# Kernel tuning notes

Hardware: AMD Instinct MI355X
Metric: run time of the kernel (lower is better)

## Reference

```python
import jax, jax.numpy as jnp
import numpy as np

N = 100000      # num_nodes
FEAT = 256      # num_features
H = 128         # hidden
C = 40          # num_classes
K = 4           # hops
RWS = 10        # random-walk samples per node
NL = 2          # nlayer
ALPHA = 0.1


def setup_inputs() -> dict:
    key = jax.random.key(0)
    ks = jax.random.split(key, 10)
    x = jax.random.normal(ks[0], (N, FEAT), dtype=jnp.float32)
    degree = jax.random.uniform(ks[1], (N,), minval=1.0, maxval=64.0, dtype=jnp.float32)
    # precomputed random-walk endpoints per layer per hop: [NL, K, N*RWS]
    ends = jax.random.randint(ks[2], (NL, K, N * RWS), 0, N, dtype=jnp.int32)
    # att init: alpha*(1-alpha)^k, last entry (1-alpha)^K, tiled per layer
    a = ALPHA * (1.0 - ALPHA) ** jnp.arange(K + 1, dtype=jnp.float32)
    a = a.at[-1].set((1.0 - ALPHA) ** K)
    att = jnp.tile(a[None, :], (NL, 1))
    def lin(k, fan_in, fan_out):
        s = 1.0 / np.sqrt(fan_in)
        return jax.random.uniform(k, (fan_in, fan_out), minval=-s, maxval=s, dtype=jnp.float32)
    W0 = lin(ks[3], FEAT, H)
    b0 = jnp.zeros((H,), dtype=jnp.float32)
    W1 = lin(ks[4], H, H)
    b1 = jnp.zeros((H,), dtype=jnp.float32)
    W2 = lin(ks[5], H, C)
    b2 = jnp.zeros((C,), dtype=jnp.float32)
    return {"x": x, "degree": degree, "ends": ends, "att": att,
            "W0": W0, "b0": b0, "W1": W1, "b1": b1, "W2": W2, "b2": b2}


def reference(x, degree, ends, att, W0, b0, W1, b1, W2, b2):
    Ws = [(W0, b0), (W1, b1)]
    starts = jnp.repeat(jnp.arange(N), RWS)          # [N*RWS] walk start node ids
    d_sqrt = jnp.sqrt(degree)                        # degree^0.5
    d_isqrt = jax.lax.rsqrt(degree)                  # degree^-0.5
    h = x
    for i in range(NL):
        W, b = Ws[i]
        h = h @ W + b                                # Linear (dropout p=0)
        mask = att[i]                                # [K+1]
        agg = h * mask[0]
        for k in range(1, K + 1):
            e = ends[i, k - 1]                       # [N*RWS] hop-k endpoints
            w = d_sqrt[starts] * d_isqrt[e]          # degree reweighting
            samp = (w[:, None] * h[e]).reshape(N, RWS, h.shape[1]).mean(axis=1)
            agg = agg + samp * mask[k]
        h = jax.nn.relu(agg)
    logits = h @ W2 + b2
    return jax.nn.log_softmax(logits, axis=1)
```

## Files before the change

kernel.cpp:

```cpp
#include <hip/hip_runtime.h>
#include <math.h>

#define NNODES 100000
#define NFEAT  256
#define HID    128
#define NCLS   40
#define KHOP   4
#define RWSAMP 10
#define KP1    5

typedef __bf16 bf16;
typedef __attribute__((ext_vector_type(8)))  __bf16 bf16x8;
typedef __attribute__((ext_vector_type(2)))  float  f32x2;
typedef __attribute__((ext_vector_type(16))) float  f32x16;

__global__ __launch_bounds__(256) void prep_w(
    const float* __restrict__ W0, const float* __restrict__ W1,
    const float* __restrict__ W2,
    bf16* __restrict__ Wt0, bf16* __restrict__ Wt1, bf16* __restrict__ Wt2)
{
    int tid = blockIdx.x * 256 + threadIdx.x;
    if (tid < 128 * 256) {
        int n = tid >> 8, k = tid & 255;
        Wt0[tid] = (bf16)W0[k * 128 + n];
    } else if (tid < 128 * 256 + 128 * 128) {
        int i = tid - 128 * 256;
        int n = i >> 7, k = i & 127;
        Wt1[i] = (bf16)W1[k * 128 + n];
    } else if (tid < 128 * 256 + 128 * 128 + 64 * 128) {
        int i = tid - (128 * 256 + 128 * 128);
        int n = i >> 7, k = i & 127;
        Wt2[i] = (n < NCLS) ? (bf16)W2[k * NCLS + n] : (bf16)0.0f;
    }
}

template<int K, bool A_BF16>
__global__ __launch_bounds__(256) void gemm_nodes(
    const void* __restrict__ Av, const bf16* __restrict__ Wt,
    const float* __restrict__ bias, unsigned char* __restrict__ F8, int M)
{
    constexpr int BK  = 128;
    constexpr int LDB = BK + 4;
    __shared__ bf16 Bs[128 * LDB];
    __shared__ bf16 As[4][32 * LDB];

    const int tid  = threadIdx.x;
    const int wv   = tid >> 6;
    const int lane = tid & 63;
    const int l31  = lane & 31;
    const int lhi  = lane >> 5;
    const int blockRow = blockIdx.x * 128;
    const int rowBase  = blockRow + wv * 32;

    const bf16*  Ab = (const bf16*)Av;
    const float* Af = (const float*)Av;

    f32x16 acc[4];
#pragma unroll
    for (int t = 0; t < 4; ++t)
#pragma unroll
        for (int r = 0; r < 16; ++r) acc[t][r] = 0.0f;

    for (int k0 = 0; k0 < K; k0 += BK) {
        if (k0) __syncthreads();
#pragma unroll 4
        for (int l = 0; l < 8; ++l) {
            int c   = tid + l * 256;
            int row = c >> 4;
            int kc  = (c & 15) * 8;
            uint4 v = *(const uint4*)(Wt + (size_t)row * K + k0 + kc);
            *(uint2*)&Bs[row * LDB + kc]     = make_uint2(v.x, v.y);
            *(uint2*)&Bs[row * LDB + kc + 4] = make_uint2(v.z, v.w);
        }
        __syncthreads();

        if (A_BF16) {
#pragma unroll 4
            for (int l = 0; l < 8; ++l) {
                int c  = lane + l * 64;
                int r  = c >> 4;
                int kc = (c & 15) * 8;
                int gr = min(rowBase + r, M - 1);
                uint4 v = *(const uint4*)(Ab + (size_t)gr * K + k0 + kc);
                *(uint2*)&As[wv][r * LDB + kc]     = make_uint2(v.x, v.y);
                *(uint2*)&As[wv][r * LDB + kc + 4] = make_uint2(v.z, v.w);
            }
        } else {
#pragma unroll 4
            for (int l = 0; l < 16; ++l) {
                int c  = lane + l * 64;
                int r  = c >> 5;
                int kc = (c & 31) * 4;
                int gr = min(rowBase + r, M - 1);
                float4 v = *(const float4*)(Af + (size_t)gr * K + k0 + kc);
                union { bf16 h[4]; uint2 u; } t4;
                t4.h[0] = (bf16)v.x; t4.h[1] = (bf16)v.y;
                t4.h[2] = (bf16)v.z; t4.h[3] = (bf16)v.w;
                *(uint2*)&As[wv][r * LDB + kc] = t4.u;
            }
        }

#pragma unroll
        for (int ks = 0; ks < BK / 16; ++ks) {
            const int ko = ks * 16 + lhi * 8;
            union { uint2 u2[2]; bf16x8 v; } ua, ub;
            ua.u2[0] = *(const uint2*)&As[wv][l31 * LDB + ko];
            ua.u2[1] = *(const uint2*)&As[wv][l31 * LDB + ko + 4];
            bf16x8 a = ua.v;
#pragma unroll
            for (int t = 0; t < 4; ++t) {
                ub.u2[0] = *(const uint2*)&Bs[(t * 32 + l31) * LDB + ko];
                ub.u2[1] = *(const uint2*)&Bs[(t * 32 + l31) * LDB + ko + 4];
                acc[t] = __builtin_amdgcn_mfma_f32_32x32x16_bf16(a, ub.v, acc[t], 0, 0, 0);
            }
        }
    }

    __syncthreads();
    unsigned* ldsq = (unsigned*)Bs;

#pragma unroll
    for (int t = 0; t < 4; ++t) {
        int col = t * 32 + l31;
        float bc = bias[col];
#pragma unroll
        for (int G = 0; G < 4; ++G) {
            float v0 = acc[t][4 * G + 0] + bc;
            float v1 = acc[t][4 * G + 1] + bc;
            float v2 = acc[t][4 * G + 2] + bc;
            float v3 = acc[t][4 * G + 3] + bc;
            int p = __builtin_amdgcn_cvt_pk_fp8_f32(v0, v1, 0, false);
            p = __builtin_amdgcn_cvt_pk_fp8_f32(v2, v3, p, true);
            ldsq[(wv * 8 + 2 * G + lhi) * 128 + col] = (unsigned)p;
        }
    }
    __syncthreads();

    {
        const int j  = tid & 31;
        const int Q0 = (tid >> 5) * 4;
#pragma unroll
        for (int qq = 0; qq < 4; ++qq) {
            int Q = Q0 + qq;
            uint4 d = *(const uint4*)&ldsq[Q * 128 + 4 * j];
            int growb = blockRow + 4 * Q;
#pragma unroll
            for (int i = 0; i < 4; ++i) {
                unsigned sel = ((unsigned)(4 + i) << 8) | (unsigned)i;
                unsigned lo = __builtin_amdgcn_perm(d.y, d.x, sel);
                unsigned hi = __builtin_amdgcn_perm(d.w, d.z, sel);
                unsigned o  = __builtin_amdgcn_perm(hi, lo, 0x05040100u);
                if (growb + i < M)
                    *(unsigned*)(F8 + (size_t)(growb + i) * 128 + 4 * j) = o;
            }
        }
    }
}

__global__ __launch_bounds__(256) void agg_relu_fp8(
    const unsigned char* __restrict__ hf8, bf16* __restrict__ hout,
    const int* __restrict__ ends, const float* __restrict__ degree,
    const float* __restrict__ att)
{
    __shared__ int2 sew[4][40];

    const int wv   = threadIdx.x >> 6;
    const int lane = threadIdx.x & 63;
    const int n    = blockIdx.x * 4 + wv;

    if (lane < KHOP * RWSAMP) {
        int k = lane / RWSAMP, s = lane - k * RWSAMP;
        int e = ends[(size_t)k * (NNODES * RWSAMP) + (size_t)n * RWSAMP + s];
        float w = att[k + 1] * (1.0f / RWSAMP) * sqrtf(degree[n]) * rsqrtf(degree[e]);
        sew[wv][lane] = make_int2(e << 7, __float_as_int(w));
    }

    const int q  = lane >> 4;
    const int c8 = (lane & 15) * 8;

    f32x2 a0 = {0.f, 0.f}, a1 = {0.f, 0.f}, a2 = {0.f, 0.f}, a3 = {0.f, 0.f};

#pragma unroll
    for (int t = 0; t < 10; ++t) {
        int2  ew   = sew[wv][4 * t + q];
        unsigned v = (unsigned)ew.x + (unsigned)c8;
        float wj   = __int_as_float(ew.y);
        f32x2 w2   = {wj, wj};
        uint2 g = *(const uint2*)(hf8 + v);
        a0 = __builtin_elementwise_fma(w2, __builtin_amdgcn_cvt_pk_f32_fp8((int)g.x, false), a0);
        a1 = __builtin_elementwise_fma(w2, __builtin_amdgcn_cvt_pk_f32_fp8((int)g.x, true),  a1);
        a2 = __builtin_elementwise_fma(w2, __builtin_amdgcn_cvt_pk_f32_fp8((int)g.y, false), a2);
        a3 = __builtin_elementwise_fma(w2, __builtin_amdgcn_cvt_pk_f32_fp8((int)g.y, true),  a3);
    }

    a0.x += __shfl_xor(a0.x, 16, 64); a0.y += __shfl_xor(a0.y, 16, 64);
    a1.x += __shfl_xor(a1.x, 16, 64); a1.y += __shfl_xor(a1.y, 16, 64);
    a2.x += __shfl_xor(a2.x, 16, 64); a2.y += __shfl_xor(a2.y, 16, 64);
    a3.x += __shfl_xor(a3.x, 16, 64); a3.y += __shfl_xor(a3.y, 16, 64);
    a0.x += __shfl_xor(a0.x, 32, 64); a0.y += __shfl_xor(a0.y, 32, 64);
    a1.x += __shfl_xor(a1.x, 32, 64); a1.y += __shfl_xor(a1.y, 32, 64);
    a2.x += __shfl_xor(a2.x, 32, 64); a2.y += __shfl_xor(a2.y, 32, 64);
    a3.x += __shfl_xor(a3.x, 32, 64); a3.y += __shfl_xor(a3.y, 32, 64);

    if (q == 0) {
        float att0 = att[0];
        f32x2 av = {att0, att0};
        unsigned vs = ((unsigned)n << 7) + (unsigned)c8;
        uint2 sv = *(const uint2*)(hf8 + vs);
        a0 = __builtin_elementwise_fma(av, __builtin_amdgcn_cvt_pk_f32_fp8((int)sv.x, false), a0);
        a1 = __builtin_elementwise_fma(av, __builtin_amdgcn_cvt_pk_f32_fp8((int)sv.x, true),  a1);
        a2 = __builtin_elementwise_fma(av, __builtin_amdgcn_cvt_pk_f32_fp8((int)sv.y, false), a2);
        a3 = __builtin_elementwise_fma(av, __builtin_amdgcn_cvt_pk_f32_fp8((int)sv.y, true),  a3);

        f32x2 z = {0.f, 0.f};
        a0 = __builtin_elementwise_max(a0, z);
        a1 = __builtin_elementwise_max(a1, z);
        a2 = __builtin_elementwise_max(a2, z);
        a3 = __builtin_elementwise_max(a3, z);

        union { bf16 h[8]; uint4 u; } st;
        st.h[0] = (bf16)a0.x; st.h[1] = (bf16)a0.y;
        st.h[2] = (bf16)a1.x; st.h[3] = (bf16)a1.y;
        st.h[4] = (bf16)a2.x; st.h[5] = (bf16)a2.y;
        st.h[6] = (bf16)a3.x; st.h[7] = (bf16)a3.y;
        *(uint4*)(hout + (size_t)n * HID + c8) = st.u;
    }
}

__global__ __launch_bounds__(256) void head_mfma(
    const bf16* __restrict__ h, const bf16* __restrict__ Wt2,
    const float* __restrict__ b2, float* __restrict__ out, int M)
{
    constexpr int K = HID, LDB = K + 8;
    __shared__ bf16 Bs[64 * LDB];

    const int tid = threadIdx.x;
    constexpr int CPR = K / 8;
    for (int f = tid; f < 64 * CPR; f += 256) {
        int row = f / CPR;
        int kc  = (f % CPR) * 8;
        *(uint4*)&Bs[row * LDB + kc] = *(const uint4*)(Wt2 + (size_t)row * K + kc);
    }
    __syncthreads();

    const int wv   = tid >> 6;
    const int lane = tid & 63;
    const int l31  = lane & 31;
    const int lhi  = lane >> 5;
    const int blockRow = blockIdx.x * 128;
    const int arow = min(blockRow + wv * 32 + l31, M - 1);

    f32x16 acc[2];
#pragma unroll
    for (int t = 0; t < 2; ++t)
#pragma unroll
        for (int r = 0; r < 16; ++r) acc[t][r] = 0.0f;

#pragma unroll
    for (int ks = 0; ks < K / 16; ++ks) {
        bf16x8 a = *(const bf16x8*)(h + (size_t)arow * K + ks * 16 + lhi * 8);
#pragma unroll
        for (int t = 0; t < 2; ++t) {
            bf16x8 b = *(const bf16x8*)&Bs[(t * 32 + l31) * LDB + ks * 16 + lhi * 8];
            acc[t] = __builtin_amdgcn_mfma_f32_32x32x16_bf16(a, b, acc[t], 0, 0, 0);
        }
    }

    const float bc0 = b2[l31];
    const float bc1 = (l31 < 8) ? b2[32 + l31] : 0.0f;

#pragma unroll
    for (int r = 0; r < 16; ++r) {
        float v0 = acc[0][r] + bc0;
        float v1 = (l31 < 8) ? (acc[1][r] + bc1) : -INFINITY;

        float m = fmaxf(v0, v1);
#pragma unroll
        for (int off = 16; off > 0; off >>= 1)
            m = fmaxf(m, __shfl_xor(m, off, 64));

        float s = __expf(v0 - m) + ((l31 < 8) ? __expf(v1 - m) : 0.0f);
#pragma unroll
        for (int off = 16; off > 0; off >>= 1)
            s += __shfl_xor(s, off, 64);

        float ls = __logf(s);
        int grow = blockRow + wv * 32 + (r & 3) + 8 * (r >> 2) + 4 * lhi;
        if (grow < M) {
            out[(size_t)grow * NCLS + l31] = v0 - m - ls;
            if (l31 < 8)
                out[(size_t)grow * NCLS + 32 + l31] = v1 - m - ls;
        }
    }
}

extern "C" void kernel_launch(void* const* d_in, const int* in_sizes, int n_in,
                              void* d_out, int out_size, void* d_ws, size_t ws_size,
                              hipStream_t stream)
{
    const float* x      = (const float*)d_in[0];
    const float* degree = (const float*)d_in[1];
    const int*   ends   = (const int*)  d_in[2];
    const float* att    = (const float*)d_in[3];
    const float* W0     = (const float*)d_in[4];
    const float* b0     = (const float*)d_in[5];
    const float* W1     = (const float*)d_in[6];
    const float* b1     = (const float*)d_in[7];
    const float* W2     = (const float*)d_in[8];
    const float* b2     = (const float*)d_in[9];
    float* out = (float*)d_out;

    bf16* hb0 = (bf16*)d_ws;
    bf16* hb1 = hb0 + (size_t)NNODES * HID;
    unsigned char* hf8 = (unsigned char*)(hb1 + (size_t)NNODES * HID);
    bf16* Wt0 = (bf16*)(hf8 + (size_t)NNODES * HID);
    bf16* Wt1 = Wt0 + 128 * 256;
    bf16* Wt2 = Wt1 + 128 * 128;

    const int prepN = 128 * 256 + 128 * 128 + 64 * 128;
    prep_w<<<(prepN + 255) / 256, 256, 0, stream>>>(W0, W1, W2, Wt0, Wt1, Wt2);

    const int gGemm = (NNODES + 127) / 128;

    gemm_nodes<NFEAT, false><<<gGemm, 256, 0, stream>>>(x, Wt0, b0, hf8, NNODES);
    agg_relu_fp8<<<NNODES / 4, 256, 0, stream>>>(hf8, hb1, ends, degree, att);
    gemm_nodes<HID, true><<<gGemm, 256, 0, stream>>>(hb1, Wt1, b1, hf8, NNODES);
    agg_relu_fp8<<<NNODES / 4, 256, 0, stream>>>(
        hf8, hb0, ends + (size_t)KHOP * NNODES * RWSAMP, degree, att + KP1);
    head_mfma<<<gGemm, 256, 0, stream>>>(hb0, Wt2, b2, out, NNODES);
}
```

Baseline: 351.3 us.

## Fuse random-walk aggregation into following GEMM and head kernels via LDS

Aggregation+ReLU is merged into the layer-1 GEMM kernel and into the classifier head kernel. Aggregated rows for a 64-node tile are staged as bf16 in shared memory instead of written to a global bf16 buffer and read back. This removes two launches and the global round trip of the intermediate activations. In exchange each wave handles 16 nodes serially in the gather phase, B operands are read straight from global memory, and half the waves idle in the head GEMM.

```diff
diff --git a/kernel.cpp b/kernel.cpp
--- a/kernel.cpp
+++ b/kernel.cpp
@@ -13,6 +13,8 @@
 typedef __attribute__((ext_vector_type(8)))  __bf16 bf16x8;
 typedef __attribute__((ext_vector_type(2)))  float  f32x2;
 typedef __attribute__((ext_vector_type(16))) float  f32x16;
+
+#define LDA 132
 
 __global__ __launch_bounds__(256) void prep_w(
     const float* __restrict__ W0, const float* __restrict__ W1,
@@ -34,13 +36,11 @@
     }
 }
 
-template<int K, bool A_BF16>
-__global__ __launch_bounds__(256) void gemm_nodes(
-    const void* __restrict__ Av, const bf16* __restrict__ Wt,
+__global__ __launch_bounds__(256) void gemm0(
+    const float* __restrict__ Af, const bf16* __restrict__ Wt,
     const float* __restrict__ bias, unsigned char* __restrict__ F8, int M)
 {
-    constexpr int BK  = 128;
-    constexpr int LDB = BK + 4;
+    constexpr int K = NFEAT, BK = 128, LDB = BK + 4;
     __shared__ bf16 Bs[128 * LDB];
     __shared__ bf16 As[4][32 * LDB];
 
@@ -51,9 +51,6 @@
     const int lhi  = lane >> 5;
     const int blockRow = blockIdx.x * 128;
     const int rowBase  = blockRow + wv * 32;
-
-    const bf16*  Ab = (const bf16*)Av;
-    const float* Af = (const float*)Av;
 
     f32x16 acc[4];
 #pragma unroll
@@ -74,30 +71,17 @@
         }
         __syncthreads();
 
-        if (A_BF16) {
 #pragma unroll 4
-            for (int l = 0; l < 8; ++l) {
-                int c  = lane + l * 64;
-                int r  = c >> 4;
-                int kc = (c & 15) * 8;
-                int gr = min(rowBase + r, M - 1);
-                uint4 v = *(const uint4*)(Ab + (size_t)gr * K + k0 + kc);
-                *(uint2*)&As[wv][r * LDB + kc]     = make_uint2(v.x, v.y);
-                *(uint2*)&As[wv][r * LDB + kc + 4] = make_uint2(v.z, v.w);
-            }
-        } else {
-#pragma unroll 4
-            for (int l = 0; l < 16; ++l) {
-                int c  = lane + l * 64;
-                int r  = c >> 5;
-                int kc = (c & 31) * 4;
-                int gr = min(rowBase + r, M - 1);
-                float4 v = *(const float4*)(Af + (size_t)gr * K + k0 + kc);
-                union { bf16 h[4]; uint2 u; } t4;
-                t4.h[0] = (bf16)v.x; t4.h[1] = (bf16)v.y;
-                t4.h[2] = (bf16)v.z; t4.h[3] = (bf16)v.w;
-                *(uint2*)&As[wv][r * LDB + kc] = t4.u;
-            }
+        for (int l = 0; l < 16; ++l) {
+            int c  = lane + l * 64;
+            int r  = c >> 5;
+            int kc = (c & 31) * 4;
+            int gr = min(rowBase + r, M - 1);
+            float4 v = *(const float4*)(Af + (size_t)gr * K + k0 + kc);
+            union { bf16 h[4]; uint2 u; } t4;
+            t4.h[0] = (bf16)v.x; t4.h[1] = (bf16)v.y;
+            t4.h[2] = (bf16)v.z; t4.h[3] = (bf16)v.w;
+            *(uint2*)&As[wv][r * LDB + kc] = t4.u;
         }
 
 #pragma unroll
@@ -157,98 +141,102 @@
     }
 }
 
-__global__ __launch_bounds__(256) void agg_relu_fp8(
-    const unsigned char* __restrict__ hf8, bf16* __restrict__ hout,
+__device__ __forceinline__ void agg_phase(
+    bf16* As, int2 (*sew)[40],
+    const unsigned char* __restrict__ f8in,
+    const int* __restrict__ ends, const float* __restrict__ degree,
+    const float* __restrict__ att, int blockRow, int wv, int lane)
+{
+    int hopoff = 0; float aw = 0.0f;
+    if (lane < KHOP * RWSAMP) {
+        int k = lane / RWSAMP, s = lane - k * RWSAMP;
+        hopoff = k * (NNODES * RWSAMP) + s;
+        aw = att[k + 1] * (1.0f / RWSAMP);
+    }
+    const float att0 = att[0];
+    const int q  = lane >> 4;
+    const int c8 = (lane & 15) * 8;
+
+    for (int i = 0; i < 16; ++i) {
+        const int n = blockRow + wv * 16 + i;
+        if (n >= NNODES) continue;
+        if (lane < KHOP * RWSAMP) {
+            int e = ends[hopoff + n * RWSAMP];
+            float w = aw * sqrtf(degree[n]) * rsqrtf(degree[e]);
+            sew[wv][lane] = make_int2(e << 7, __float_as_int(w));
+        }
+
+        f32x2 a0 = {0.f, 0.f}, a1 = {0.f, 0.f}, a2 = {0.f, 0.f}, a3 = {0.f, 0.f};
+#pragma unroll
+        for (int t = 0; t < 10; ++t) {
+            int2  ew   = sew[wv][4 * t + q];
+            unsigned v = (unsigned)ew.x + (unsigned)c8;
+            float wj   = __int_as_float(ew.y);
+            f32x2 w2   = {wj, wj};
+            uint2 g = *(const uint2*)(f8in + v);
+            a0 = __builtin_elementwise_fma(w2, __builtin_amdgcn_cvt_pk_f32_fp8((int)g.x, false), a0);
+            a1 = __builtin_elementwise_fma(w2, __builtin_amdgcn_cvt_pk_f32_fp8((int)g.x, true),  a1);
+            a2 = __builtin_elementwise_fma(w2, __builtin_amdgcn_cvt_pk_f32_fp8((int)g.y, false), a2);
+            a3 = __builtin_elementwise_fma(w2, __builtin_amdgcn_cvt_pk_f32_fp8((int)g.y, true),  a3);
+        }
+
+        a0.x += __shfl_xor(a0.x, 16, 64); a0.y += __shfl_xor(a0.y, 16, 64);
+        a1.x += __shfl_xor(a1.x, 16, 64); a1.y += __shfl_xor(a1.y, 16, 64);
+        a2.x += __shfl_xor(a2.x, 16, 64); a2.y += __shfl_xor(a2.y, 16, 64);
+        a3.x += __shfl_xor(a3.x, 16, 64); a3.y += __shfl_xor(a3.y, 16, 64);
+        a0.x += __shfl_xor(a0.x, 32, 64); a0.y += __shfl_xor(a0.y, 32, 64);
+        a1.x += __shfl_xor(a1.x, 32, 64); a1.y += __shfl_xor(a1.y, 32, 64);
+        a2.x += __shfl_xor(a2.x, 32, 64); a2.y += __shfl_xor(a2.y, 32, 64);
+        a3.x += __shfl_xor(a3.x, 32, 64); a3.y += __shfl_xor(a3.y, 32, 64);
+
+        if (q == 0) {
+            f32x2 av = {att0, att0};
+            unsigned vs = ((unsigned)n << 7) + (unsigned)c8;
+            uint2 sv = *(const uint2*)(f8in + vs);
+            a0 = __builtin_elementwise_fma(av, __builtin_amdgcn_cvt_pk_f32_fp8((int)sv.x, false), a0);
+            a1 = __builtin_elementwise_fma(av, __builtin_amdgcn_cvt_pk_f32_fp8((int)sv.x, true),  a1);
+            a2 = __builtin_elementwise_fma(av, __builtin_amdgcn_cvt_pk_f32_fp8((int)sv.y, false), a2);
+            a3 = __builtin_elementwise_fma(av, __builtin_amdgcn_cvt_pk_f32_fp8((int)sv.y, true),  a3);
+
+            f32x2 z = {0.f, 0.f};
+            a0 = __builtin_elementwise_max(a0, z);
+            a1 = __builtin_elementwise_max(a1, z);
+            a2 = __builtin_elementwise_max(a2, z);
+            a3 = __builtin_elementwise_max(a3, z);
+
+            union { bf16 h[8]; uint2 u[2]; } st;
+            st.h[0] = (bf16)a0.x; st.h[1] = (bf16)a0.y;
+            st.h[2] = (bf16)a1.x; st.h[3] = (bf16)a1.y;
+            st.h[4] = (bf16)a2.x; st.h[5] = (bf16)a2.y;
+            st.h[6] = (bf16)a3.x; st.h[7] = (bf16)a3.y;
+            int r = wv * 16 + i;
+            *(uint2*)&As[r * LDA + c8]     = st.u[0];
+            *(uint2*)&As[r * LDA + c8 + 4] = st.u[1];
+        }
+    }
+}
+
+__global__ __launch_bounds__(256) void layer_fused(
+    const unsigned char* __restrict__ f8in, const bf16* __restrict__ Wt,
+    const float* __restrict__ bias, unsigned char* __restrict__ F8out,
     const int* __restrict__ ends, const float* __restrict__ degree,
     const float* __restrict__ att)
 {
+    __shared__ bf16 As[64 * LDA];
     __shared__ int2 sew[4][40];
 
-    const int wv   = threadIdx.x >> 6;
-    const int lane = threadIdx.x & 63;
-    const int n    = blockIdx.x * 4 + wv;
-
-    if (lane < KHOP * RWSAMP) {
-        int k = lane / RWSAMP, s = lane - k * RWSAMP;
-        int e = ends[(size_t)k * (NNODES * RWSAMP) + (size_t)n * RWSAMP + s];
-        float w = att[k + 1] * (1.0f / RWSAMP) * sqrtf(degree[n]) * rsqrtf(degree[e]);
-        sew[wv][lane] = make_int2(e << 7, __float_as_int(w));
-    }
-
-    const int q  = lane >> 4;
-    const int c8 = (lane & 15) * 8;
-
-    f32x2 a0 = {0.f, 0.f}, a1 = {0.f, 0.f}, a2 = {0.f, 0.f}, a3 = {0.f, 0.f};
-
-#pragma unroll
-    for (int t = 0; t < 10; ++t) {
-        int2  ew   = sew[wv][4 * t + q];
-        unsigned v = (unsigned)ew.x + (unsigned)c8;
-        float wj   = __int_as_float(ew.y);
-        f32x2 w2   = {wj, wj};
-        uint2 g = *(const uint2*)(hf8 + v);
-        a0 = __builtin_elementwise_fma(w2, __builtin_amdgcn_cvt_pk_f32_fp8((int)g.x, false), a0);
-        a1 = __builtin_elementwise_fma(w2, __builtin_amdgcn_cvt_pk_f32_fp8((int)g.x, true),  a1);
-        a2 = __builtin_elementwise_fma(w2, __builtin_amdgcn_cvt_pk_f32_fp8((int)g.y, false), a2);
-        a3 = __builtin_elementwise_fma(w2, __builtin_amdgcn_cvt_pk_f32_fp8((int)g.y, true),  a3);
-    }
-
-    a0.x += __shfl_xor(a0.x, 16, 64); a0.y += __shfl_xor(a0.y, 16, 64);
-    a1.x += __shfl_xor(a1.x, 16, 64); a1.y += __shfl_xor(a1.y, 16, 64);
-    a2.x += __shfl_xor(a2.x, 16, 64); a2.y += __shfl_xor(a2.y, 16, 64);
-    a3.x += __shfl_xor(a3.x, 16, 64); a3.y += __shfl_xor(a3.y, 16, 64);
-    a0.x += __shfl_xor(a0.x, 32, 64); a0.y += __shfl_xor(a0.y, 32, 64);
-    a1.x += __shfl_xor(a1.x, 32, 64); a1.y += __shfl_xor(a1.y, 32, 64);
-    a2.x += __shfl_xor(a2.x, 32, 64); a2.y += __shfl_xor(a2.y, 32, 64);
-    a3.x += __shfl_xor(a3.x, 32, 64); a3.y += __shfl_xor(a3.y, 32, 64);
-
-    if (q == 0) {
-        float att0 = att[0];
-        f32x2 av = {att0, att0};
-        unsigned vs = ((unsigned)n << 7) + (unsigned)c8;
-        uint2 sv = *(const uint2*)(hf8 + vs);
-        a0 = __builtin_elementwise_fma(av, __builtin_amdgcn_cvt_pk_f32_fp8((int)sv.x, false), a0);
-        a1 = __builtin_elementwise_fma(av, __builtin_amdgcn_cvt_pk_f32_fp8((int)sv.x, true),  a1);
-        a2 = __builtin_elementwise_fma(av, __builtin_amdgcn_cvt_pk_f32_fp8((int)sv.y, false), a2);
-        a3 = __builtin_elementwise_fma(av, __builtin_amdgcn_cvt_pk_f32_fp8((int)sv.y, true),  a3);
-
-        f32x2 z = {0.f, 0.f};
-        a0 = __builtin_elementwise_max(a0, z);
-        a1 = __builtin_elementwise_max(a1, z);
-        a2 = __builtin_elementwise_max(a2, z);
-        a3 = __builtin_elementwise_max(a3, z);
-
-        union { bf16 h[8]; uint4 u; } st;
-        st.h[0] = (bf16)a0.x; st.h[1] = (bf16)a0.y;
-        st.h[2] = (bf16)a1.x; st.h[3] = (bf16)a1.y;
-        st.h[4] = (bf16)a2.x; st.h[5] = (bf16)a2.y;
-        st.h[6] = (bf16)a3.x; st.h[7] = (bf16)a3.y;
-        *(uint4*)(hout + (size_t)n * HID + c8) = st.u;
-    }
-}
-
-__global__ __launch_bounds__(256) void head_mfma(
-    const bf16* __restrict__ h, const bf16* __restrict__ Wt2,
-    const float* __restrict__ b2, float* __restrict__ out, int M)
-{
-    constexpr int K = HID, LDB = K + 8;
-    __shared__ bf16 Bs[64 * LDB];
-
-    const int tid = threadIdx.x;
-    constexpr int CPR = K / 8;
-    for (int f = tid; f < 64 * CPR; f += 256) {
-        int row = f / CPR;
-        int kc  = (f % CPR) * 8;
-        *(uint4*)&Bs[row * LDB + kc] = *(const uint4*)(Wt2 + (size_t)row * K + kc);
-    }
-    __syncthreads();
-
+    const int tid  = threadIdx.x;
     const int wv   = tid >> 6;
     const int lane = tid & 63;
-    const int l31  = lane & 31;
-    const int lhi  = lane >> 5;
-    const int blockRow = blockIdx.x * 128;
-    const int arow = min(blockRow + wv * 32 + l31, M - 1);
+    const int blockRow = blockIdx.x * 64;
+
+    agg_phase(As, sew, f8in, ends, degree, att, blockRow, wv, lane);
+    __syncthreads();
+
+    const int l31 = lane & 31;
+    const int lhi = lane >> 5;
+    const int sp  = wv & 1;
+    const int t0  = (wv >> 1) * 2;
 
     f32x16 acc[2];
 #pragma unroll
@@ -257,12 +245,96 @@
         for (int r = 0; r < 16; ++r) acc[t][r] = 0.0f;
 
 #pragma unroll
-    for (int ks = 0; ks < K / 16; ++ks) {
-        bf16x8 a = *(const bf16x8*)(h + (size_t)arow * K + ks * 16 + lhi * 8);
-#pragma unroll
-        for (int t = 0; t < 2; ++t) {
-            bf16x8 b = *(const bf16x8*)&Bs[(t * 32 + l31) * LDB + ks * 16 + lhi * 8];
-            acc[t] = __builtin_amdgcn_mfma_f32_32x32x16_bf16(a, b, acc[t], 0, 0, 0);
+    for (int ks = 0; ks < 8; ++ks) {
+        const int ko = ks * 16 + lhi * 8;
+        union { uint2 u2[2]; bf16x8 v; } ua;
+        ua.u2[0] = *(const uint2*)&As[(sp * 32 + l31) * LDA + ko];
+        ua.u2[1] = *(const uint2*)&As[(sp * 32 + l31) * LDA + ko + 4];
+#pragma unroll
+        for (int tt = 0; tt < 2; ++tt) {
+            bf16x8 b = *(const bf16x8*)(Wt + (size_t)((t0 + tt) * 32 + l31) * HID + ko);
+            acc[tt] = __builtin_amdgcn_mfma_f32_32x32x16_bf16(ua.v, b, acc[tt], 0, 0, 0);
+        }
+    }
+    __syncthreads();
+
+    unsigned* ldsq = (unsigned*)As;
+#pragma unroll
+    for (int tt = 0; tt < 2; ++tt) {
+        int col = (t0 + tt) * 32 + l31;
+        float bc = bias[col];
+#pragma unroll
+        for (int G = 0; G < 4; ++G) {
+            float v0 = acc[tt][4 * G + 0] + bc;
+            float v1 = acc[tt][4 * G + 1] + bc;
+            float v2 = acc[tt][4 * G + 2] + bc;
+            float v3 = acc[tt][4 * G + 3] + bc;
+            int p = __builtin_amdgcn_cvt_pk_fp8_f32(v0, v1, 0, false);
+            p = __builtin_amdgcn_cvt_pk_fp8_f32(v2, v3, p, true);
+            ldsq[(sp * 8 + 2 * G + lhi) * 128 + col] = (unsigned)p;
+        }
+    }
+    __syncthreads();
+
+    {
+        const int j = tid & 31;
+#pragma unroll
+        for (int qq = 0; qq < 2; ++qq) {
+            int Q = (tid >> 5) * 2 + qq;
+            uint4 d = *(const uint4*)&ldsq[Q * 128 + 4 * j];
+            int growb = blockRow + 4 * Q;
+#pragma unroll
+            for (int i = 0; i < 4; ++i) {
+                unsigned sel = ((unsigned)(4 + i) << 8) | (unsigned)i;
+                unsigned lo = __builtin_amdgcn_perm(d.y, d.x, sel);
+                unsigned hi = __builtin_amdgcn_perm(d.w, d.z, sel);
+                unsigned o  = __builtin_amdgcn_perm(hi, lo, 0x05040100u);
+                if (growb + i < NNODES)
+                    *(unsigned*)(F8out + (size_t)(growb + i) * 128 + 4 * j) = o;
+            }
+        }
+    }
+}
+
+__global__ __launch_bounds__(256) void head_fused(
+    const unsigned char* __restrict__ f8in, const bf16* __restrict__ Wt2,
+    const float* __restrict__ b2, float* __restrict__ out,
+    const int* __restrict__ ends, const float* __restrict__ degree,
+    const float* __restrict__ att)
+{
+    __shared__ bf16 As[64 * LDA];
+    __shared__ int2 sew[4][40];
+
+    const int tid  = threadIdx.x;
+    const int wv   = tid >> 6;
+    const int lane = tid & 63;
+    const int blockRow = blockIdx.x * 64;
+
+    agg_phase(As, sew, f8in, ends, degree, att, blockRow, wv, lane);
+    __syncthreads();
+
+    if (wv >= 2) return;
+
+    const int l31 = lane & 31;
+    const int lhi = lane >> 5;
+    const int sp  = wv;
+
+    f32x16 acc[2];
+#pragma unroll
+    for (int t = 0; t < 2; ++t)
+#pragma unroll
+        for (int r = 0; r < 16; ++r) acc[t][r] = 0.0f;
+
+#pragma unroll
+    for (int ks = 0; ks < 8; ++ks) {
+        const int ko = ks * 16 + lhi * 8;
+        union { uint2 u2[2]; bf16x8 v; } ua;
+        ua.u2[0] = *(const uint2*)&As[(sp * 32 + l31) * LDA + ko];
+        ua.u2[1] = *(const uint2*)&As[(sp * 32 + l31) * LDA + ko + 4];
+#pragma unroll
+        for (int tt = 0; tt < 2; ++tt) {
+            bf16x8 b = *(const bf16x8*)(Wt2 + (size_t)(tt * 32 + l31) * HID + ko);
+            acc[tt] = __builtin_amdgcn_mfma_f32_32x32x16_bf16(ua.v, b, acc[tt], 0, 0, 0);
         }
     }
 
@@ -285,8 +357,8 @@
             s += __shfl_xor(s, off, 64);
 
         float ls = __logf(s);
-        int grow = blockRow + wv * 32 + (r & 3) + 8 * (r >> 2) + 4 * lhi;
-        if (grow < M) {
+        int grow = blockRow + sp * 32 + (r & 3) + 8 * (r >> 2) + 4 * lhi;
+        if (grow < NNODES) {
             out[(size_t)grow * NCLS + l31] = v0 - m - ls;
             if (l31 < 8)
                 out[(size_t)grow * NCLS + 32 + l31] = v1 - m - ls;
@@ -310,22 +382,20 @@
     const float* b2     = (const float*)d_in[9];
     float* out = (float*)d_out;
 
-    bf16* hb0 = (bf16*)d_ws;
-    bf16* hb1 = hb0 + (size_t)NNODES * HID;
-    unsigned char* hf8 = (unsigned char*)(hb1 + (size_t)NNODES * HID);
-    bf16* Wt0 = (bf16*)(hf8 + (size_t)NNODES * HID);
+    unsigned char* f8a = (unsigned char*)d_ws;
+    unsigned char* f8b = f8a + (size_t)NNODES * HID;
+    bf16* Wt0 = (bf16*)(f8b + (size_t)NNODES * HID);
     bf16* Wt1 = Wt0 + 128 * 256;
     bf16* Wt2 = Wt1 + 128 * 128;
 
     const int prepN = 128 * 256 + 128 * 128 + 64 * 128;
     prep_w<<<(prepN + 255) / 256, 256, 0, stream>>>(W0, W1, W2, Wt0, Wt1, Wt2);
 
-    const int gGemm = (NNODES + 127) / 128;
-
-    gemm_nodes<NFEAT, false><<<gGemm, 256, 0, stream>>>(x, Wt0, b0, hf8, NNODES);
-    agg_relu_fp8<<<NNODES / 4, 256, 0, stream>>>(hf8, hb1, ends, degree, att);
-    gemm_nodes<HID, true><<<gGemm, 256, 0, stream>>>(hb1, Wt1, b1, hf8, NNODES);
-    agg_relu_fp8<<<NNODES / 4, 256, 0, stream>>>(
-        hf8, hb0, ends + (size_t)KHOP * NNODES * RWSAMP, degree, att + KP1);
-    head_mfma<<<gGemm, 256, 0, stream>>>(hb0, Wt2, b2, out, NNODES);
-}
+    const int gG0 = (NNODES + 127) / 128;
+    const int gF  = (NNODES + 63) / 64;
+
+    gemm0<<<gG0, 256, 0, stream>>>(x, Wt0, b0, f8a, NNODES);
+    layer_fused<<<gF, 256, 0, stream>>>(f8a, Wt1, b1, f8b, ends, degree, att);
+    head_fused<<<gF, 256, 0, stream>>>(
+        f8b, Wt2, b2, out, ends + (size_t)KHOP * NNODES * RWSAMP, degree, att + KP1);
+}
```

Result: slower. 388.4 us (+10.6%).
